# Kernel optimization log

Measured on AMD Instinct MI355X. Metric: run time of the kernel, lower is better.

Reference implementation:

```python
import jax, jax.numpy as jnp
import numpy as np

B, N, IN_DIM = 2, 2048, 512
D_MODEL, N_HEADS, N_CLASSES = 1024, 16, 1024


def sin_pos_encoding(n, d):
    # Matches SinPositionalEncoding buffer pe[:n]
    pos = jnp.arange(n, dtype=jnp.float32)[:, None]
    div = jnp.exp(jnp.arange(0, d, 2, dtype=jnp.float32) * (-np.log(10000.0) / d))
    pe = jnp.zeros((n, d), dtype=jnp.float32)
    pe = pe.at[:, 0::2].set(jnp.sin(pos * div))
    pe = pe.at[:, 1::2].set(jnp.cos(pos * div))
    return pe


def setup_inputs() -> dict:
    key = jax.random.key(0)
    ks = jax.random.split(key, 9)
    s_emb = (2.0 / (IN_DIM + D_MODEL)) ** 0.5
    s_qk = (2.0 / (2 * D_MODEL)) ** 0.5
    s_v = (2.0 / (D_MODEL + 1)) ** 0.5
    s_o = (2.0 / (N_HEADS + D_MODEL)) ** 0.5
    s_dec = (2.0 / (D_MODEL + N_CLASSES)) ** 0.5
    return {
        'X': jax.random.normal(ks[0], (B, N, IN_DIM), dtype=jnp.float32),
        'emb_w': jax.random.normal(ks[1], (IN_DIM, D_MODEL), dtype=jnp.float32) * s_emb,
        'emb_b': jax.random.normal(ks[2], (D_MODEL,), dtype=jnp.float32) * 0.01,
        'Wq': jax.random.normal(ks[3], (N_HEADS, D_MODEL, D_MODEL), dtype=jnp.float32) * s_qk,
        'Wk': jax.random.normal(ks[4], (N_HEADS, D_MODEL, D_MODEL), dtype=jnp.float32) * s_qk,
        'Wv': jax.random.normal(ks[5], (N_HEADS, D_MODEL, 1), dtype=jnp.float32) * s_v,
        'Wo': jax.random.normal(ks[6], (N_HEADS, D_MODEL), dtype=jnp.float32) * s_o,
        'dec_w': jax.random.normal(ks[7], (D_MODEL, N_CLASSES), dtype=jnp.float32) * s_dec,
        'dec_b': jax.random.normal(ks[8], (N_CLASSES,), dtype=jnp.float32) * 0.01,
    }


def reference(X, emb_w, emb_b, Wq, Wk, Wv, Wo, dec_w, dec_b):
    b, n, _ = X.shape
    d = emb_w.shape[1]
    h = X @ emb_w + emb_b                       # [b, n, d]
    h = h + sin_pos_encoding(n, d)[None]        # positional encoding
    Q = jnp.einsum('bnd,hde->bhne', h, Wq)      # [b, H, n, d]
    K = jnp.einsum('bnd,hde->bhne', h, Wk)      # [b, H, n, d]
    V = jnp.einsum('bnd,hdv->bhnv', h, Wv)      # [b, H, n, 1]
    scores = jnp.einsum('bhqe,bhke->bhqk', Q, K) / jnp.sqrt(jnp.float32(d))
    # mask[:, 0] = 1 is applied MULTIPLICATIVELY before softmax: column 0 -> 0
    scores = scores.at[..., 0].set(0.0)
    attn = jax.nn.softmax(scores, axis=-1)      # [b, H, n, n]
    ctx = jnp.einsum('bhqk,bhkv->bhqv', attn, V)  # [b, H, n, 1]
    ctx = jnp.transpose(ctx, (0, 2, 1, 3)).reshape(b, n, -1)  # [b, n, H]
    out = ctx @ Wo                              # [b, n, d]
    out = out @ dec_w + dec_b                   # [b, n, n_classes]
    return out
```

## Files before the change

kernel.cpp:

```cpp
#include <hip/hip_runtime.h>
#include <cstdint>

typedef __attribute__((ext_vector_type(8))) short bf16x8;
typedef __attribute__((ext_vector_type(4))) float f32x4;

#define B_ 2
#define N_ 2048
#define IN_DIM_ 512
#define D_ 1024
#define H_ 16

__device__ __forceinline__ unsigned short f2bf(float f) {
  uint32_t u = __float_as_uint(f);
  u = u + 0x7fffu + ((u >> 16) & 1u);
  return (unsigned short)(u >> 16);
}
__device__ __forceinline__ float bf2f(unsigned short b) {
  return __uint_as_float(((uint32_t)b) << 16);
}

__device__ __forceinline__ void gll16(const void* g, void* l) {
  __builtin_amdgcn_global_load_lds(
      (const __attribute__((address_space(1))) uint32_t*)g,
      (__attribute__((address_space(3))) uint32_t*)l, 16, 0, 0);
}

__global__ __launch_bounds__(256) void cast_bf16(const float* __restrict__ X,
                                                 unsigned short* __restrict__ O, int n) {
  int i = (blockIdx.x * 256 + threadIdx.x) * 4;
  if (i + 3 < n) {
    f32x4 v = *(const f32x4*)(X + i);
    uint32_t p0 = (uint32_t)f2bf(v[0]) | ((uint32_t)f2bf(v[1]) << 16);
    uint32_t p1 = (uint32_t)f2bf(v[2]) | ((uint32_t)f2bf(v[3]) << 16);
    *(uint32_t*)(O + i) = p0;
    *(uint32_t*)(O + i + 2) = p1;
  }
}

__global__ __launch_bounds__(256) void cast_bf16x2(const float* __restrict__ X0,
                                                   const float* __restrict__ X1,
                                                   unsigned short* __restrict__ O0,
                                                   unsigned short* __restrict__ O1, int n) {
  int i = (blockIdx.x * 256 + threadIdx.x) * 4;
  const bool second = (i >= n);
  const int j = second ? i - n : i;
  const float* X = second ? X1 : X0;
  unsigned short* O = second ? O1 : O0;
  f32x4 v = *(const f32x4*)(X + j);
  uint32_t p0 = (uint32_t)f2bf(v[0]) | ((uint32_t)f2bf(v[1]) << 16);
  uint32_t p1 = (uint32_t)f2bf(v[2]) | ((uint32_t)f2bf(v[3]) << 16);
  *(uint32_t*)(O + j) = p0;
  *(uint32_t*)(O + j + 2) = p1;
}

__global__ __launch_bounds__(256) void transpose_cast(const float* __restrict__ W,
                                                      unsigned short* __restrict__ WT,
                                                      int K, int N) {
  __shared__ float t[32][33];
  const int tx = threadIdx.x, ty = threadIdx.y;
  const int x = blockIdx.x * 32 + tx;
  const int y = blockIdx.y * 32 + ty;
  #pragma unroll
  for (int i = 0; i < 4; ++i)
    t[ty + i * 8][tx] = W[(size_t)(y + i * 8) * N + x];
  __syncthreads();
  const int ox = blockIdx.y * 32 + tx;
  #pragma unroll
  for (int i = 0; i < 4; ++i) {
    const int oy = blockIdx.x * 32 + ty + i * 8;
    WT[(size_t)oy * K + ox] = f2bf(t[tx][ty + i * 8]);
  }
}

__global__ __launch_bounds__(256) void gemm_embed(
    const unsigned short* __restrict__ Xbf, const unsigned short* __restrict__ EbT,
    const float* __restrict__ emb_b, unsigned short* __restrict__ Hbf) {
  const int tid = threadIdx.x, l = tid & 63, w = tid >> 6;
  const int wm = w >> 1, wn = w & 1;
  const int bm = blockIdx.y * 128, bn = blockIdx.x * 128;
  __shared__ unsigned short As[128 * 32], Bs[128 * 32];
  const unsigned short* Ab = Xbf + (size_t)bm * IN_DIM_;
  const unsigned short* Bb = EbT + (size_t)bn * IN_DIM_;
  f32x4 acc[4][4] = {};
  const int lr = l >> 2, lc = (l & 3) * 8;
  for (int k0 = 0; k0 < IN_DIM_; k0 += 32) {
    #pragma unroll
    for (int i = 0; i < 2; ++i) {
      const int c = w * 2 + i;
      gll16(Ab + (size_t)(c * 16 + lr) * IN_DIM_ + k0 + lc, As + c * 512);
      gll16(Bb + (size_t)(c * 16 + lr) * IN_DIM_ + k0 + lc, Bs + c * 512);
    }
    __syncthreads();
    bf16x8 af[4], bfr[4];
    #pragma unroll
    for (int f = 0; f < 4; ++f) {
      af[f]  = *(const bf16x8*)(As + (wm * 64 + f * 16 + (l & 15)) * 32 + (l >> 4) * 8);
      bfr[f] = *(const bf16x8*)(Bs + (wn * 64 + f * 16 + (l & 15)) * 32 + (l >> 4) * 8);
    }
    #pragma unroll
    for (int fr = 0; fr < 4; ++fr)
      #pragma unroll
      for (int fc = 0; fc < 4; ++fc)
        acc[fr][fc] = __builtin_amdgcn_mfma_f32_16x16x32_bf16(af[fr], bfr[fc], acc[fr][fc], 0, 0, 0);
    __syncthreads();
  }
  const float kF = -0.017988946039015983f;
  #pragma unroll
  for (int fr = 0; fr < 4; ++fr) {
    #pragma unroll
    for (int fc = 0; fc < 4; ++fc) {
      const int col = bn + wn * 64 + fc * 16 + (l & 15);
      const float eb = emb_b[col];
      const float fac = expf((float)(col >> 1) * kF);
      #pragma unroll
      for (int j = 0; j < 4; ++j) {
        const int row = bm + wm * 64 + fr * 16 + (l >> 4) * 4 + j;
        const float pos = (float)(row & (N_ - 1));
        const float ang = pos * fac;
        const float pe = (col & 1) ? cosf(ang) : sinf(ang);
        float v = acc[fr][fc][j] + eb + pe;
        float o = __shfl_xor(v, 1);
        unsigned short mb = f2bf(v), ob = f2bf(o);
        uint32_t pk = (l & 1) ? ((uint32_t)ob | ((uint32_t)mb << 16))
                              : ((uint32_t)mb | ((uint32_t)ob << 16));
        const bool mine = (l & 1) ? (j >= 2) : (j < 2);
        if (mine)
          *(uint32_t*)(Hbf + (size_t)row * D_ + (col & ~1)) = pk;
      }
    }
  }
}

__global__ __launch_bounds__(256) void gemm_nt(
    const unsigned short* __restrict__ A, const unsigned short* __restrict__ Bm,
    unsigned short* __restrict__ O, int K, long aZ, long bZ, long oZ, int swz) {
  int bx = blockIdx.x, by = blockIdx.y, bz = blockIdx.z;
  if (swz) {
    const int nx = gridDim.x, ny = gridDim.y;
    const int nwg = nx * ny * gridDim.z;
    const int bid = bx + nx * (by + ny * bz);
    const int wid = (bid & 7) * (nwg >> 3) + (bid >> 3);
    bx = wid % nx;
    const int rest = wid / nx;
    by = rest % ny;
    bz = rest / ny;
  }
  const int z = bz;
  const int tid = threadIdx.x, l = tid & 63, w = tid >> 6;
  const int wm = w >> 1, wn = w & 1;
  const int bm = by * 128, bn = bx * 128;
  const int ldo = gridDim.x * 128;
  __shared__ unsigned short As[2 * 128 * 32], Bs[2 * 128 * 32];
  const unsigned short* Ab = A + (size_t)z * aZ + (size_t)bm * K;
  const unsigned short* Bb = Bm + (size_t)z * bZ + (size_t)bn * K;
  f32x4 acc[4][4] = {};
  const int lr = l >> 2, lc = (l & 3) * 8;
  for (int k0 = 0; k0 < K; k0 += 64) {
    #pragma unroll
    for (int half = 0; half < 2; ++half) {
      #pragma unroll
      for (int i = 0; i < 2; ++i) {
        const int c = w * 2 + i;
        gll16(Ab + (size_t)(c * 16 + lr) * K + k0 + half * 32 + lc,
              As + half * 4096 + c * 512);
        gll16(Bb + (size_t)(c * 16 + lr) * K + k0 + half * 32 + lc,
              Bs + half * 4096 + c * 512);
      }
    }
    __syncthreads();
    #pragma unroll
    for (int half = 0; half < 2; ++half) {
      bf16x8 af[4], bfr[4];
      #pragma unroll
      for (int f = 0; f < 4; ++f) {
        af[f]  = *(const bf16x8*)(As + half * 4096 + (wm * 64 + f * 16 + (l & 15)) * 32 + (l >> 4) * 8);
        bfr[f] = *(const bf16x8*)(Bs + half * 4096 + (wn * 64 + f * 16 + (l & 15)) * 32 + (l >> 4) * 8);
      }
      #pragma unroll
      for (int fr = 0; fr < 4; ++fr)
        #pragma unroll
        for (int fc = 0; fc < 4; ++fc)
          acc[fr][fc] = __builtin_amdgcn_mfma_f32_16x16x32_bf16(af[fr], bfr[fc], acc[fr][fc], 0, 0, 0);
    }
    __syncthreads();
  }
  unsigned short* obase = O + (size_t)z * oZ;
  #pragma unroll
  for (int fr = 0; fr < 4; ++fr) {
    #pragma unroll
    for (int fc = 0; fc < 4; ++fc) {
      const int col = bn + wn * 64 + fc * 16 + (l & 15);
      #pragma unroll
      for (int j = 0; j < 4; ++j) {
        const int row = bm + wm * 64 + fr * 16 + (l >> 4) * 4 + j;
        float v = acc[fr][fc][j];
        float o = __shfl_xor(v, 1);
        unsigned short mb = f2bf(v), ob = f2bf(o);
        uint32_t pk = (l & 1) ? ((uint32_t)ob | ((uint32_t)mb << 16))
                              : ((uint32_t)mb | ((uint32_t)ob << 16));
        const bool mine = (l & 1) ? (j >= 2) : (j < 2);
        if (mine)
          *(uint32_t*)(obase + (size_t)row * ldo + (col & ~1)) = pk;
      }
    }
  }
}

__global__ __launch_bounds__(256) void v_wodec_kernel(
    const unsigned short* __restrict__ Hbf, const float* __restrict__ Wv,
    float* __restrict__ V, const float* __restrict__ Wo,
    const float* __restrict__ dec_w, float* __restrict__ M) {
  if (blockIdx.x < 1024) {
    const int l = threadIdx.x & 63, w = threadIdx.x >> 6;
    const int ng = blockIdx.x * 4 + w;
    const int b = ng >> 11, n = ng & (N_ - 1);
    const unsigned short* hr = Hbf + (size_t)ng * D_;
    float hv[16];
    #pragma unroll
    for (int i = 0; i < 2; ++i) {
      bf16x8 x = *(const bf16x8*)(hr + l * 16 + i * 8);
      #pragma unroll
      for (int j = 0; j < 8; ++j) hv[i * 8 + j] = bf2f((unsigned short)x[j]);
    }
    for (int h = 0; h < H_; ++h) {
      const float* wr = Wv + (size_t)h * D_ + l * 16;
      float s = 0.f;
      #pragma unroll
      for (int i = 0; i < 4; ++i) {
        f32x4 w4 = *(const f32x4*)(wr + i * 4);
        s += hv[i*4+0]*w4[0] + hv[i*4+1]*w4[1] + hv[i*4+2]*w4[2] + hv[i*4+3]*w4[3];
      }
      #pragma unroll
      for (int m = 1; m < 64; m <<= 1) s += __shfl_xor(s, m);
      if (l == 0) V[((size_t)b * H_ + h) * N_ + n] = s;
    }
  } else {
    const int idx = (blockIdx.x - 1024) * 256 + threadIdx.x;
    const int h = idx >> 10, c = idx & 1023;
    float s = 0.f;
    #pragma unroll 4
    for (int d = 0; d < D_; ++d) s += Wo[h * D_ + d] * dec_w[(size_t)d * 1024 + c];
    M[idx] = s;
  }
}

__global__ __launch_bounds__(256) void score_flash(
    const unsigned short* __restrict__ G, const unsigned short* __restrict__ Hb,
    const float* __restrict__ V, float* __restrict__ Pp) {
  const int bid = blockIdx.x;
  const int wid = (bid & 7) * 512 + (bid >> 3);
  const int kt = wid & 15, qt = (wid >> 4) & 15, h = wid >> 8;
  const int tid = threadIdx.x, l = tid & 63, w = tid >> 6;
  const int wm = w >> 1, wn = w & 1;
  __shared__ unsigned short As[2 * 128 * 32], Bs[2 * 128 * 32];
  __shared__ float sb[2][128][2];
  const unsigned short* Ab = G + ((size_t)h * N_ + qt * 128) * D_;
  const unsigned short* Bb = Hb + (size_t)(kt * 128) * D_;
  const float* Vf = V + (size_t)h * N_;
  f32x4 acc[4][4] = {};
  const int lr = l >> 2, lc = (l & 3) * 8;
  for (int k0 = 0; k0 < D_; k0 += 64) {
    #pragma unroll
    for (int half = 0; half < 2; ++half) {
      #pragma unroll
      for (int i = 0; i < 2; ++i) {
        const int c = w * 2 + i;
        gll16(Ab + (size_t)(c * 16 + lr) * D_ + k0 + half * 32 + lc,
              As + half * 4096 + c * 512);
        gll16(Bb + (size_t)(c * 16 + lr) * D_ + k0 + half * 32 + lc,
              Bs + half * 4096 + c * 512);
      }
    }
    __syncthreads();
    #pragma unroll
    for (int half = 0; half < 2; ++half) {
      bf16x8 af[4], bfr[4];
      #pragma unroll
      for (int f = 0; f < 4; ++f) {
        af[f]  = *(const bf16x8*)(As + half * 4096 + (wm * 64 + f * 16 + (l & 15)) * 32 + (l >> 4) * 8);
        bfr[f] = *(const bf16x8*)(Bs + half * 4096 + (wn * 64 + f * 16 + (l & 15)) * 32 + (l >> 4) * 8);
      }
      #pragma unroll
      for (int fr = 0; fr < 4; ++fr)
        #pragma unroll
        for (int fc = 0; fc < 4; ++fc)
          acc[fr][fc] = __builtin_amdgcn_mfma_f32_16x16x32_bf16(af[fr], bfr[fc], acc[fr][fc], 0, 0, 0);
    }
    __syncthreads();
  }
  float vv[4];
  #pragma unroll
  for (int fc = 0; fc < 4; ++fc)
    vv[fc] = Vf[kt * 128 + wn * 64 + fc * 16 + (l & 15)];
  #pragma unroll
  for (int fr = 0; fr < 4; ++fr) {
    #pragma unroll
    for (int j = 0; j < 4; ++j) {
      float s4[4];
      #pragma unroll
      for (int fc = 0; fc < 4; ++fc) s4[fc] = acc[fr][fc][j] * 0.03125f;
      if (kt == 0 && wn == 0 && (l & 15) == 0) s4[0] = 0.0f;
      float ps = 0.f, pv = 0.f;
      #pragma unroll
      for (int fc = 0; fc < 4; ++fc) {
        const float e = __expf(s4[fc] - 8.0f);
        ps += e; pv += e * vv[fc];
      }
      ps += __shfl_xor(ps, 1); pv += __shfl_xor(pv, 1);
      ps += __shfl_xor(ps, 2); pv += __shfl_xor(pv, 2);
      ps += __shfl_xor(ps, 4); pv += __shfl_xor(pv, 4);
      ps += __shfl_xor(ps, 8); pv += __shfl_xor(pv, 8);
      if ((l & 15) == 0) {
        const int r = wm * 64 + fr * 16 + (l >> 4) * 4 + j;
        sb[wn][r][0] = ps; sb[wn][r][1] = pv;
      }
    }
  }
  __syncthreads();
  if (tid < 128) {
    const int r = tid;
    float* p = Pp + (((size_t)h * 16 + kt) * N_ + qt * 128 + r) * 2;
    p[0] = sb[0][r][0] + sb[1][r][0];
    p[1] = sb[0][r][1] + sb[1][r][1];
  }
}

__global__ __launch_bounds__(256) void merge16(const float* __restrict__ Pp,
                                               float* __restrict__ ctx) {
  const int idx = blockIdx.x * 256 + threadIdx.x;
  const int h = idx >> 11, q = idx & (N_ - 1);
  float L = 0.f, O = 0.f;
  #pragma unroll
  for (int kt = 0; kt < 16; ++kt) {
    const float* p = Pp + (((size_t)h * 16 + kt) * N_ + q) * 2;
    L += p[0]; O += p[1];
  }
  ctx[(size_t)q * H_ + h] = O / L;
}

__global__ __launch_bounds__(256) void final_kernel(
    const float* __restrict__ ctx, const float* __restrict__ M,
    const float* __restrict__ dec_b, float* __restrict__ out) {
  const int idx = blockIdx.x * 256 + threadIdx.x;
  const int c = idx & 1023;
  const float* cr = ctx + (size_t)(idx >> 10) * H_;
  float s = dec_b[c];
  #pragma unroll
  for (int h = 0; h < H_; ++h) s += cr[h] * M[h * 1024 + c];
  out[idx] = s;
}

extern "C" void kernel_launch(void* const* d_in, const int* in_sizes, int n_in,
                              void* d_out, int out_size, void* d_ws, size_t ws_size,
                              hipStream_t stream) {
  const float* X     = (const float*)d_in[0];
  const float* emb_w = (const float*)d_in[1];
  const float* emb_b = (const float*)d_in[2];
  const float* Wq    = (const float*)d_in[3];
  const float* Wk    = (const float*)d_in[4];
  const float* Wv    = (const float*)d_in[5];
  const float* Wo    = (const float*)d_in[6];
  const float* dec_b = (const float*)d_in[8];
  const float* dec_w = (const float*)d_in[7];
  float* out = (float*)d_out;
  (void)in_sizes; (void)n_in; (void)out_size;

  char* ws = (char*)d_ws;
  unsigned short* Hbf = (unsigned short*)(ws);
  unsigned short* Wkq = (unsigned short*)(ws + ((size_t)8 << 20));
  float* Vb  = (float*)(ws + ((size_t)40 << 20));
  float* ctx = (float*)(ws + ((size_t)40 << 20) + ((size_t)256 << 10));
  float* Mw  = (float*)(ws + ((size_t)40 << 20) + ((size_t)512 << 10));
  char* S = ws + ((size_t)41 << 20);
  unsigned short* Xbf  = (unsigned short*)(S);
  unsigned short* EbT  = (unsigned short*)(S + ((size_t)4 << 20));
  unsigned short* Wqbf = (unsigned short*)(S);
  unsigned short* Wkbf = (unsigned short*)(S + ((size_t)32 << 20));
  unsigned short* G    = (unsigned short*)(S);
  float* Pp = (float*)d_out;

  const size_t need = ((size_t)41 << 20) + ((size_t)64 << 20);
  if (ws_size < need) return;

  cast_bf16<<<2048, 256, 0, stream>>>(X, Xbf, B_ * N_ * IN_DIM_);
  transpose_cast<<<dim3(32, 16, 1), dim3(32, 8), 0, stream>>>(emb_w, EbT, IN_DIM_, D_);
  gemm_embed<<<dim3(8, 32), 256, 0, stream>>>(Xbf, EbT, emb_b, Hbf);
  cast_bf16x2<<<32768, 256, 0, stream>>>(Wq, Wk, Wqbf, Wkbf, H_ * D_ * D_);
  gemm_nt<<<dim3(8, 8, 16), 256, 0, stream>>>(Wkbf, Wqbf, Wkq, D_,
                                              (long)D_ * D_, (long)D_ * D_, (long)D_ * D_, 1);
  v_wodec_kernel<<<1088, 256, 0, stream>>>(Hbf, Wv, Vb, Wo, dec_w, Mw);

  for (int b = 0; b < B_; ++b) {
    const unsigned short* Hb = Hbf + (size_t)b * N_ * D_;
    gemm_nt<<<dim3(8, 16, 16), 256, 0, stream>>>(Hb, Wkq, G, D_,
                                                 0L, (long)D_ * D_, (long)N_ * D_, 1);
    score_flash<<<4096, 256, 0, stream>>>(G, Hb, Vb + (size_t)b * H_ * N_, Pp);
    merge16<<<128, 256, 0, stream>>>(Pp, ctx + (size_t)b * N_ * H_);
  }
  final_kernel<<<16384, 256, 0, stream>>>(ctx, Mw, dec_b, out);
}
```

Measured before the change: 843.4 us.

## Enlarge score_flash tile to 256x128 with full-row per-wave ownership

The score kernel's query tile grows from 128 to 256 rows, and each wave now owns 64 full rows across all 128 key columns instead of a 64x64 quadrant. Each wave computes its row sums of exp and exp·V alone, so the shared-memory cross-wave reduction and the final barrier go away, and each block writes partials straight to global memory. The larger tile halves the grid and cuts reloading of the key tile per query, which reduces global and LDS traffic per MFMA. In exchange, registers per thread rise with 32 accumulator fragments and 8 B fragments, which may lower occupancy, and each wave reads all 128 B rows from LDS.

```diff
diff --git a/kernel.cpp b/kernel.cpp
--- a/kernel.cpp
+++ b/kernel.cpp
@@ -248,80 +248,78 @@
     const unsigned short* __restrict__ G, const unsigned short* __restrict__ Hb,
     const float* __restrict__ V, float* __restrict__ Pp) {
   const int bid = blockIdx.x;
-  const int wid = (bid & 7) * 512 + (bid >> 3);
-  const int kt = wid & 15, qt = (wid >> 4) & 15, h = wid >> 8;
+  const int wid = (bid & 7) * 256 + (bid >> 3);
+  const int kt = wid & 15, qt = (wid >> 4) & 7, h = wid >> 7;
   const int tid = threadIdx.x, l = tid & 63, w = tid >> 6;
-  const int wm = w >> 1, wn = w & 1;
-  __shared__ unsigned short As[2 * 128 * 32], Bs[2 * 128 * 32];
-  __shared__ float sb[2][128][2];
-  const unsigned short* Ab = G + ((size_t)h * N_ + qt * 128) * D_;
+  __shared__ unsigned short As[2 * 256 * 32];
+  __shared__ unsigned short Bs[2 * 128 * 32];
+  const unsigned short* Ab = G + ((size_t)h * N_ + qt * 256) * D_;
   const unsigned short* Bb = Hb + (size_t)(kt * 128) * D_;
   const float* Vf = V + (size_t)h * N_;
-  f32x4 acc[4][4] = {};
+  f32x4 acc[4][8] = {};
   const int lr = l >> 2, lc = (l & 3) * 8;
   for (int k0 = 0; k0 < D_; k0 += 64) {
     #pragma unroll
     for (int half = 0; half < 2; ++half) {
       #pragma unroll
-      for (int i = 0; i < 2; ++i) {
-        const int c = w * 2 + i;
-        gll16(Ab + (size_t)(c * 16 + lr) * D_ + k0 + half * 32 + lc,
-              As + half * 4096 + c * 512);
-        gll16(Bb + (size_t)(c * 16 + lr) * D_ + k0 + half * 32 + lc,
-              Bs + half * 4096 + c * 512);
+      for (int i = 0; i < 6; ++i) {
+        const int c = w * 6 + i;
+        if (c < 16) {
+          gll16(Ab + (size_t)(c * 16 + lr) * D_ + k0 + half * 32 + lc,
+                As + half * 8192 + c * 512);
+        } else {
+          const int u = c - 16;
+          gll16(Bb + (size_t)(u * 16 + lr) * D_ + k0 + half * 32 + lc,
+                Bs + half * 4096 + u * 512);
+        }
       }
     }
     __syncthreads();
     #pragma unroll
     for (int half = 0; half < 2; ++half) {
-      bf16x8 af[4], bfr[4];
-      #pragma unroll
-      for (int f = 0; f < 4; ++f) {
-        af[f]  = *(const bf16x8*)(As + half * 4096 + (wm * 64 + f * 16 + (l & 15)) * 32 + (l >> 4) * 8);
-        bfr[f] = *(const bf16x8*)(Bs + half * 4096 + (wn * 64 + f * 16 + (l & 15)) * 32 + (l >> 4) * 8);
-      }
+      bf16x8 af[4], bfr[8];
+      #pragma unroll
+      for (int fr = 0; fr < 4; ++fr)
+        af[fr] = *(const bf16x8*)(As + half * 8192 + (w * 64 + fr * 16 + (l & 15)) * 32 + (l >> 4) * 8);
+      #pragma unroll
+      for (int f = 0; f < 8; ++f)
+        bfr[f] = *(const bf16x8*)(Bs + half * 4096 + (f * 16 + (l & 15)) * 32 + (l >> 4) * 8);
       #pragma unroll
       for (int fr = 0; fr < 4; ++fr)
         #pragma unroll
-        for (int fc = 0; fc < 4; ++fc)
-          acc[fr][fc] = __builtin_amdgcn_mfma_f32_16x16x32_bf16(af[fr], bfr[fc], acc[fr][fc], 0, 0, 0);
-    }
-    __syncthreads();
-  }
-  float vv[4];
-  #pragma unroll
-  for (int fc = 0; fc < 4; ++fc)
-    vv[fc] = Vf[kt * 128 + wn * 64 + fc * 16 + (l & 15)];
+        for (int f = 0; f < 8; ++f)
+          acc[fr][f] = __builtin_amdgcn_mfma_f32_16x16x32_bf16(af[fr], bfr[f], acc[fr][f], 0, 0, 0);
+    }
+    __syncthreads();
+  }
+  float vv[8];
+  #pragma unroll
+  for (int f = 0; f < 8; ++f)
+    vv[f] = Vf[kt * 128 + f * 16 + (l & 15)];
   #pragma unroll
   for (int fr = 0; fr < 4; ++fr) {
     #pragma unroll
     for (int j = 0; j < 4; ++j) {
-      float s4[4];
-      #pragma unroll
-      for (int fc = 0; fc < 4; ++fc) s4[fc] = acc[fr][fc][j] * 0.03125f;
-      if (kt == 0 && wn == 0 && (l & 15) == 0) s4[0] = 0.0f;
+      float s8[8];
+      #pragma unroll
+      for (int f = 0; f < 8; ++f) s8[f] = acc[fr][f][j] * 0.03125f;
+      if (kt == 0 && (l & 15) == 0) s8[0] = 0.0f;
       float ps = 0.f, pv = 0.f;
       #pragma unroll
-      for (int fc = 0; fc < 4; ++fc) {
-        const float e = __expf(s4[fc] - 8.0f);
-        ps += e; pv += e * vv[fc];
+      for (int f = 0; f < 8; ++f) {
+        const float e = __expf(s8[f] - 8.0f);
+        ps += e; pv += e * vv[f];
       }
       ps += __shfl_xor(ps, 1); pv += __shfl_xor(pv, 1);
       ps += __shfl_xor(ps, 2); pv += __shfl_xor(pv, 2);
       ps += __shfl_xor(ps, 4); pv += __shfl_xor(pv, 4);
       ps += __shfl_xor(ps, 8); pv += __shfl_xor(pv, 8);
       if ((l & 15) == 0) {
-        const int r = wm * 64 + fr * 16 + (l >> 4) * 4 + j;
-        sb[wn][r][0] = ps; sb[wn][r][1] = pv;
-      }
-    }
-  }
-  __syncthreads();
-  if (tid < 128) {
-    const int r = tid;
-    float* p = Pp + (((size_t)h * 16 + kt) * N_ + qt * 128 + r) * 2;
-    p[0] = sb[0][r][0] + sb[1][r][0];
-    p[1] = sb[0][r][1] + sb[1][r][1];
+        const int q = qt * 256 + w * 64 + fr * 16 + (l >> 4) * 4 + j;
+        float* p = Pp + (((size_t)h * 16 + kt) * N_ + q) * 2;
+        p[0] = ps; p[1] = pv;
+      }
+    }
   }
 }
 
@@ -394,7 +392,7 @@
     const unsigned short* Hb = Hbf + (size_t)b * N_ * D_;
     gemm_nt<<<dim3(8, 16, 16), 256, 0, stream>>>(Hb, Wkq, G, D_,
                                                  0L, (long)D_ * D_, (long)N_ * D_, 1);
-    score_flash<<<4096, 256, 0, stream>>>(G, Hb, Vb + (size_t)b * H_ * N_, Pp);
+    score_flash<<<2048, 256, 0, stream>>>(G, Hb, Vb + (size_t)b * H_ * N_, Pp);
     merge16<<<128, 256, 0, stream>>>(Pp, ctx + (size_t)b * N_ * H_);
   }
   final_kernel<<<16384, 256, 0, stream>>>(ctx, Mw, dec_b, out);
```

Measured after the change: 790.6 us. -6.3%, faster.

## Enlarge score tile to 256x256 with double-buffered swizzled LDS pipeline

Applied to the files above, without the earlier changes.

Reworks the score kernel to use 512 threads per block, each block computing a 256x256 query-by-key tile instead of 128x128. The K loop becomes double-buffered: global-to-LDS loads for the next 64-wide K slice are interleaved with MFMA work on the current one, using explicit vmcnt waits, barriers and setprio, and LDS columns are XOR-swizzled to avoid bank conflicts. The larger tile improves operand reuse and halves the number of partial softmax results, so the merge kernel now combines 8 partials instead of 16. The cost is 128 KB of dynamic shared memory per block, which limits occupancy, and hand-tuned wait counts that are fragile to scheduling.

```diff
diff --git a/kernel.cpp b/kernel.cpp
--- a/kernel.cpp
+++ b/kernel.cpp
@@ -244,62 +244,112 @@
   }
 }
 
-__global__ __launch_bounds__(256) void score_flash(
+__global__ __launch_bounds__(512, 2) void score_flash(
     const unsigned short* __restrict__ G, const unsigned short* __restrict__ Hb,
     const float* __restrict__ V, float* __restrict__ Pp) {
+  extern __shared__ unsigned short KQ[];
   const int bid = blockIdx.x;
-  const int wid = (bid & 7) * 512 + (bid >> 3);
-  const int kt = wid & 15, qt = (wid >> 4) & 15, h = wid >> 8;
-  const int tid = threadIdx.x, l = tid & 63, w = tid >> 6;
-  const int wm = w >> 1, wn = w & 1;
-  __shared__ unsigned short As[2 * 128 * 32], Bs[2 * 128 * 32];
-  __shared__ float sb[2][128][2];
-  const unsigned short* Ab = G + ((size_t)h * N_ + qt * 128) * D_;
-  const unsigned short* Bb = Hb + (size_t)(kt * 128) * D_;
+  const int wid = (bid & 7) * 128 + (bid >> 3);
+  const int kt = wid & 7, qt = (wid >> 3) & 7, h = wid >> 6;
+  const int tid = threadIdx.x;
+  const int l = tid & 63, l15 = l & 15, l7 = l & 7, lq = l >> 4;
+  const int wv = tid >> 6, wm = wv >> 2, wn = wv & 3;
+  const unsigned short* Ab = G + ((size_t)h * N_ + qt * 256) * D_;
+  const unsigned short* Bb = Hb + (size_t)(kt * 256) * D_;
   const float* Vf = V + (size_t)h * N_;
-  f32x4 acc[4][4] = {};
-  const int lr = l >> 2, lc = (l & 3) * 8;
-  for (int k0 = 0; k0 < D_; k0 += 64) {
-    #pragma unroll
-    for (int half = 0; half < 2; ++half) {
-      #pragma unroll
-      for (int i = 0; i < 2; ++i) {
-        const int c = w * 2 + i;
-        gll16(Ab + (size_t)(c * 16 + lr) * D_ + k0 + half * 32 + lc,
-              As + half * 4096 + c * 512);
-        gll16(Bb + (size_t)(c * 16 + lr) * D_ + k0 + half * 32 + lc,
-              Bs + half * 4096 + c * 512);
-      }
-    }
-    __syncthreads();
-    #pragma unroll
-    for (int half = 0; half < 2; ++half) {
-      bf16x8 af[4], bfr[4];
-      #pragma unroll
-      for (int f = 0; f < 4; ++f) {
-        af[f]  = *(const bf16x8*)(As + half * 4096 + (wm * 64 + f * 16 + (l & 15)) * 32 + (l >> 4) * 8);
-        bfr[f] = *(const bf16x8*)(Bs + half * 4096 + (wn * 64 + f * 16 + (l & 15)) * 32 + (l >> 4) * 8);
-      }
-      #pragma unroll
-      for (int fr = 0; fr < 4; ++fr)
+
+  const int srow = tid >> 3, spc = tid & 7, scol = (spc ^ (srow & 7)) * 8;
+  auto stageU = [&](const unsigned short* src, int rowBase, int k0, unsigned short* ldsU) {
+    gll16(src + (size_t)(rowBase + srow) * D_ + k0 + scol, ldsU + tid * 8);
+  };
+
+  float vv[4];
+  #pragma unroll
+  for (int fc = 0; fc < 4; ++fc)
+    vv[fc] = Vf[kt * 256 + wn * 64 + fc * 16 + l15];
+
+  {
+    unsigned short* A0 = KQ;
+    unsigned short* B0 = KQ + 16384;
+    stageU(Bb, 0, 0, B0); stageU(Bb, 64, 0, B0 + 4096);
+    stageU(Bb, 128, 0, B0 + 8192); stageU(Bb, 192, 0, B0 + 12288);
+    stageU(Ab, 0, 0, A0); stageU(Ab, 128, 0, A0 + 8192);
+    stageU(Ab, 64, 0, A0 + 4096); stageU(Ab, 192, 0, A0 + 12288);
+  }
+  __builtin_amdgcn_sched_barrier(0);
+  asm volatile("s_waitcnt vmcnt(2)" ::: "memory");
+  __builtin_amdgcn_s_barrier();
+  __builtin_amdgcn_sched_barrier(0);
+
+  f32x4 acc[8][4] = {};
+  const int arow0 = wm * 128 + l15;
+  const int brow0 = wn * 64 + l15;
+
+  for (int t = 0; t < 16; ++t) {
+    unsigned short* Acur = KQ + (t & 1) * 32768;
+    unsigned short* Bcur = Acur + 16384;
+    unsigned short* Anxt = KQ + ((t & 1) ^ 1) * 32768;
+    unsigned short* Bnxt = Anxt + 16384;
+    const int k0n = (t + 1) * 64;
+    const bool more = (t < 15);
+    bf16x8 bfr[4][2];
+    #pragma unroll
+    for (int r = 0; r < 4; ++r) {
+      if (r == 0) {
         #pragma unroll
         for (int fc = 0; fc < 4; ++fc)
-          acc[fr][fc] = __builtin_amdgcn_mfma_f32_16x16x32_bf16(af[fr], bfr[fc], acc[fr][fc], 0, 0, 0);
-    }
-    __syncthreads();
-  }
-  float vv[4];
-  #pragma unroll
-  for (int fc = 0; fc < 4; ++fc)
-    vv[fc] = Vf[kt * 128 + wn * 64 + fc * 16 + (l & 15)];
-  #pragma unroll
-  for (int fr = 0; fr < 4; ++fr) {
+          #pragma unroll
+          for (int kh = 0; kh < 2; ++kh)
+            bfr[fc][kh] = *(const bf16x8*)(Bcur + (brow0 + fc * 16) * 64 +
+                                           (((kh * 4 + lq) ^ l7) * 8));
+      }
+      bf16x8 af[2][2];
+      #pragma unroll
+      for (int i = 0; i < 2; ++i)
+        #pragma unroll
+        for (int kh = 0; kh < 2; ++kh)
+          af[i][kh] = *(const bf16x8*)(Acur + (arow0 + (2 * r + i) * 16) * 64 +
+                                       (((kh * 4 + lq) ^ l7) * 8));
+      if (more) {
+        if (r == 0)      { stageU(Bb, 0, k0n, Bnxt);        stageU(Bb, 64, k0n, Bnxt + 4096); }
+        else if (r == 1) { stageU(Bb, 128, k0n, Bnxt + 8192); stageU(Bb, 192, k0n, Bnxt + 12288); }
+        else if (r == 2) { stageU(Ab, 0, k0n, Anxt);        stageU(Ab, 128, k0n, Anxt + 8192); }
+        else             { stageU(Ab, 64, k0n, Anxt + 4096); stageU(Ab, 192, k0n, Anxt + 12288); }
+      }
+      __builtin_amdgcn_sched_barrier(0);
+      if (r == 1) {
+        if (t == 15) asm volatile("s_waitcnt vmcnt(0)" ::: "memory");
+        else         asm volatile("s_waitcnt vmcnt(4)" ::: "memory");
+      }
+      if (r == 3 && more) asm volatile("s_waitcnt vmcnt(2)" ::: "memory");
+      __builtin_amdgcn_s_barrier();
+      __builtin_amdgcn_sched_barrier(0);
+      __builtin_amdgcn_s_setprio(1);
+      #pragma unroll
+      for (int i = 0; i < 2; ++i)
+        #pragma unroll
+        for (int fc = 0; fc < 4; ++fc)
+          #pragma unroll
+          for (int kh = 0; kh < 2; ++kh)
+            acc[2 * r + i][fc] = __builtin_amdgcn_mfma_f32_16x16x32_bf16(
+                af[i][kh], bfr[fc][kh], acc[2 * r + i][fc], 0, 0, 0);
+      __builtin_amdgcn_s_setprio(0);
+      __builtin_amdgcn_sched_barrier(0);
+      __builtin_amdgcn_s_barrier();
+      __builtin_amdgcn_sched_barrier(0);
+    }
+  }
+
+  __syncthreads();
+  float* sb = (float*)KQ;
+  #pragma unroll
+  for (int fr = 0; fr < 8; ++fr) {
     #pragma unroll
     for (int j = 0; j < 4; ++j) {
       float s4[4];
       #pragma unroll
       for (int fc = 0; fc < 4; ++fc) s4[fc] = acc[fr][fc][j] * 0.03125f;
-      if (kt == 0 && wn == 0 && (l & 15) == 0) s4[0] = 0.0f;
+      if (kt == 0 && wn == 0 && l15 == 0) s4[0] = 0.0f;
       float ps = 0.f, pv = 0.f;
       #pragma unroll
       for (int fc = 0; fc < 4; ++fc) {
@@ -310,29 +360,32 @@
       ps += __shfl_xor(ps, 2); pv += __shfl_xor(pv, 2);
       ps += __shfl_xor(ps, 4); pv += __shfl_xor(pv, 4);
       ps += __shfl_xor(ps, 8); pv += __shfl_xor(pv, 8);
-      if ((l & 15) == 0) {
-        const int r = wm * 64 + fr * 16 + (l >> 4) * 4 + j;
-        sb[wn][r][0] = ps; sb[wn][r][1] = pv;
+      if (l15 == 0) {
+        const int q = wm * 128 + fr * 16 + lq * 4 + j;
+        sb[(q * 4 + wn) * 2 + 0] = ps;
+        sb[(q * 4 + wn) * 2 + 1] = pv;
       }
     }
   }
   __syncthreads();
-  if (tid < 128) {
-    const int r = tid;
-    float* p = Pp + (((size_t)h * 16 + kt) * N_ + qt * 128 + r) * 2;
-    p[0] = sb[0][r][0] + sb[1][r][0];
-    p[1] = sb[0][r][1] + sb[1][r][1];
-  }
-}
-
-__global__ __launch_bounds__(256) void merge16(const float* __restrict__ Pp,
-                                               float* __restrict__ ctx) {
+  if (tid < 256) {
+    const int q = tid;
+    float L = 0.f, O = 0.f;
+    #pragma unroll
+    for (int n = 0; n < 4; ++n) { L += sb[(q * 4 + n) * 2]; O += sb[(q * 4 + n) * 2 + 1]; }
+    float* p = Pp + (((size_t)h * 8 + kt) * N_ + qt * 256 + q) * 2;
+    p[0] = L; p[1] = O;
+  }
+}
+
+__global__ __launch_bounds__(256) void merge8(const float* __restrict__ Pp,
+                                              float* __restrict__ ctx) {
   const int idx = blockIdx.x * 256 + threadIdx.x;
   const int h = idx >> 11, q = idx & (N_ - 1);
   float L = 0.f, O = 0.f;
   #pragma unroll
-  for (int kt = 0; kt < 16; ++kt) {
-    const float* p = Pp + (((size_t)h * 16 + kt) * N_ + q) * 2;
+  for (int kt = 0; kt < 8; ++kt) {
+    const float* p = Pp + (((size_t)h * 8 + kt) * N_ + q) * 2;
     L += p[0]; O += p[1];
   }
   ctx[(size_t)q * H_ + h] = O / L;
@@ -394,8 +447,8 @@
     const unsigned short* Hb = Hbf + (size_t)b * N_ * D_;
     gemm_nt<<<dim3(8, 16, 16), 256, 0, stream>>>(Hb, Wkq, G, D_,
                                                  0L, (long)D_ * D_, (long)N_ * D_, 1);
-    score_flash<<<4096, 256, 0, stream>>>(G, Hb, Vb + (size_t)b * H_ * N_, Pp);
-    merge16<<<128, 256, 0, stream>>>(Pp, ctx + (size_t)b * N_ * H_);
+    score_flash<<<1024, 512, 131072, stream>>>(G, Hb, Vb + (size_t)b * H_ * N_, Pp);
+    merge8<<<128, 256, 0, stream>>>(Pp, ctx + (size_t)b * N_ * H_);
   }
   final_kernel<<<16384, 256, 0, stream>>>(ctx, Mw, dec_b, out);
 }
```

After: 756.1 us (median of 2 runs). 1.12x faster.
